# Optimization experiments

Hardware: AMD Instinct MI355X
Metric: run time of the kernel (lower is better)

The kernel has to match this reference:

```python
import jax, jax.numpy as jnp
import numpy as np

N_NODES = 50000


def _spmm(edge_index, edge_vals, dense):
    """Sparse [N,N] @ dense [N,D] via gather + segment-sum.
    edge_index[0] = row (dst), edge_index[1] = col (src)."""
    dst, src = edge_index[0], edge_index[1]
    msgs = edge_vals[:, None] * dense[src]  # [E, D]
    return jax.ops.segment_sum(msgs, dst, num_segments=N_NODES)


def setup_inputs() -> dict:
    key = jax.random.key(0)
    ks = jax.random.split(key, 8)
    N, D_IN, D_OUT, E = N_NODES, 128, 128, 800000
    x = jax.random.normal(ks[0], (N, D_IN), dtype=jnp.float32)
    # glorot init for weights
    scale = jnp.sqrt(6.0 / (D_IN + D_OUT)).astype(jnp.float32)
    W0 = jax.random.uniform(ks[1], (D_IN, D_OUT), jnp.float32, -scale, scale)
    W1 = jax.random.uniform(ks[2], (D_IN, D_OUT), jnp.float32, -scale, scale)
    bias = jnp.zeros((D_OUT,), dtype=jnp.float32)
    edge_vals0 = jax.random.uniform(ks[3], (E,), dtype=jnp.float32)
    edge_vals1 = jax.random.uniform(ks[4], (E,), dtype=jnp.float32)
    edge_index0 = jax.random.randint(ks[5], (2, E), 0, N, dtype=jnp.int32)
    edge_index1 = jax.random.randint(ks[6], (2, E), 0, N, dtype=jnp.int32)
    return {"x": x, "W0": W0, "W1": W1, "bias": bias,
            "edge_vals0": edge_vals0, "edge_vals1": edge_vals1,
            "edge_index0": edge_index0, "edge_index1": edge_index1}


def reference(x, W0, W1, bias, edge_vals0, edge_vals1, edge_index0, edge_index1):
    # dropout with rate 0 == identity (self.dropout unset in source snippet)
    pre0 = x @ W0  # [N, D_out]
    pre1 = x @ W1
    out = _spmm(edge_index0, edge_vals0, pre0) + _spmm(edge_index1, edge_vals1, pre1)
    out = out + bias
    return jax.nn.relu(out)
```

## Files before the change

### kernel.cpp

```cpp
#include <hip/hip_runtime.h>
#include <hip/hip_bf16.h>


#define BROWS 32
#define NBUCK 1563
#define BCAP 704
#define ACAP (2 * BCAP)
#define FT 4096
#define PREROWS 65536

typedef __attribute__((ext_vector_type(8))) short bf16x8;
typedef __attribute__((ext_vector_type(4))) float f32x4;

__device__ inline unsigned short f2bf(float f) {
    union { float f; unsigned u; } v; v.f = f;
    unsigned r = v.u + 0x7fff + ((v.u >> 16) & 1);
    return (unsigned short)(r >> 16);
}

__global__ __launch_bounds__(256) void convert_w_kernel(
    const float* __restrict__ W0, const float* __restrict__ W1,
    unsigned short* __restrict__ wt0, unsigned short* __restrict__ wt1,
    int* __restrict__ cur, int ncur)
{
    if (blockIdx.x >= 2) {
        int half = (ncur + 1) / 2;
        int base = (blockIdx.x - 2) * half;
        for (int i = threadIdx.x; i < half; i += 256)
            if (base + i < ncur) cur[base + i] = 0;
        return;
    }
    const float* __restrict__ W = blockIdx.x ? W1 : W0;
    unsigned short* __restrict__ wt = blockIdx.x ? wt1 : wt0;
    for (int i = threadIdx.x; i < 128 * 128; i += 256) {
        int k = i >> 7, n = i & 127;
        wt[n * 128 + k] = f2bf(W[i]);
    }
}

__global__ __launch_bounds__(512) void gemm_fused_kernel(
    const float* __restrict__ x,
    const unsigned short* __restrict__ wt0,
    const unsigned short* __restrict__ wt1,
    unsigned short* __restrict__ pre,
    int N)
{
    __shared__ short ctile[8][16][40];

    const int w = threadIdx.x >> 6;
    const int lane = threadIdx.x & 63;
    const int adj = w >> 2;
    const int wq = w & 3;
    const int m0 = blockIdx.x * 16;
    const unsigned short* __restrict__ wt = adj ? wt1 : wt0;
    unsigned short* __restrict__ po = pre + (size_t)adj * PREROWS * 128;
    const int l15 = lane & 15;
    const int quad = lane >> 4;
    const int nA = wq * 32 + l15;

    f32x4 c0 = {0.f, 0.f, 0.f, 0.f};
    f32x4 c1 = {0.f, 0.f, 0.f, 0.f};
#pragma unroll
    for (int k0 = 0; k0 < 128; k0 += 32) {
        const float* xp = &x[(m0 + l15) * 128 + k0 + quad * 8];
        float4 v0 = *(const float4*)xp;
        float4 v1 = *(const float4*)(xp + 4);
        bf16x8 a;
        ((short*)&a)[0] = (short)f2bf(v0.x);
        ((short*)&a)[1] = (short)f2bf(v0.y);
        ((short*)&a)[2] = (short)f2bf(v0.z);
        ((short*)&a)[3] = (short)f2bf(v0.w);
        ((short*)&a)[4] = (short)f2bf(v1.x);
        ((short*)&a)[5] = (short)f2bf(v1.y);
        ((short*)&a)[6] = (short)f2bf(v1.z);
        ((short*)&a)[7] = (short)f2bf(v1.w);
        bf16x8 b0 = *(const bf16x8*)&wt[nA * 128 + k0 + quad * 8];
        bf16x8 b1 = *(const bf16x8*)&wt[(nA + 16) * 128 + k0 + quad * 8];
        c0 = __builtin_amdgcn_mfma_f32_16x16x32_bf16(a, b0, c0, 0, 0, 0);
        c1 = __builtin_amdgcn_mfma_f32_16x16x32_bf16(a, b1, c1, 0, 0, 0);
    }

#pragma unroll
    for (int i = 0; i < 4; ++i) {
        ctile[w][quad * 4 + i][l15]      = (short)f2bf(c0[i]);
        ctile[w][quad * 4 + i][16 + l15] = (short)f2bf(c1[i]);
    }
    const int rr = lane >> 2, cg = (lane & 3) * 8;
    ushort4 s0 = *(ushort4*)&ctile[w][rr][cg];
    ushort4 s1 = *(ushort4*)&ctile[w][rr][cg + 4];
    int row = m0 + rr;
    *(ushort4*)&po[row * 128 + wq * 32 + cg] = s0;
    *(ushort4*)&po[row * 128 + wq * 32 + cg + 4] = s1;
}

__global__ __launch_bounds__(1024) void fill4_kernel(
    const int* __restrict__ ei0, const int* __restrict__ ei1,
    const float* __restrict__ ev0, const float* __restrict__ ev1,
    int* __restrict__ cur, int2* __restrict__ recs, int E)
{
    const int a = blockIdx.y;
    const int* __restrict__ ei = a ? ei1 : ei0;
    const float* __restrict__ ev = a ? ev1 : ev0;

    __shared__ int lcnt[NBUCK];
    __shared__ int gbase[NBUCK];
    __shared__ int glim[NBUCK];
    for (int k = threadIdx.x; k < NBUCK; k += 1024) lcnt[k] = 0;
    __syncthreads();

    const int e0 = blockIdx.x * FT;
    unsigned ds[4];
    float val[4];
    short rank[4];
#pragma unroll
    for (int j = 0; j < 4; ++j) {
        int e = e0 + j * 1024 + threadIdx.x;
        if (e < E) {
            int d = ei[e];
            int s = ei[E + e];
            ds[j] = ((unsigned)d << 16) | (unsigned)s;
            val[j] = ev[e];
            rank[j] = (short)atomicAdd(&lcnt[d >> 5], 1);
        } else ds[j] = 0xffffffffu;
    }
    __syncthreads();

    for (int k = threadIdx.x; k < NBUCK; k += 1024) {
        int c = lcnt[k];
        int base = 0, lim = 0;
        if (c > 0) {
            int bin = k * 2 + a;
            int b0 = atomicAdd(&cur[bin], c);
            lim = BCAP - b0; if (lim < 0) lim = 0;
            base = bin * BCAP + b0;
        }
        gbase[k] = base;
        glim[k] = lim;
    }
    __syncthreads();

#pragma unroll
    for (int j = 0; j < 4; ++j) {
        if (ds[j] != 0xffffffffu) {
            int key = ds[j] >> 21;
            int r = rank[j];
            if (r < glim[key]) {
                int rl = (ds[j] >> 16) & 31;
                recs[gbase[key] + r] =
                    make_int2((rl << 17) | (a << 16) | (ds[j] & 0xffff),
                              __float_as_int(val[j]));
            }
        }
    }
}

__global__ __launch_bounds__(256, 6) void aggregate9_kernel(
    const int* __restrict__ cur, const int2* __restrict__ recs,
    const unsigned short* __restrict__ pre,
    const float* __restrict__ bias,
    float* __restrict__ out, int N)
{
    __shared__ int2 srec[ACAP];
    __shared__ int2 srt[ACAP];
    __shared__ int lcnt[32];
    __shared__ int lstart[32];
    __shared__ int lcur[32];

    const int b = blockIdx.x;
    const int tid = threadIdx.x;

    int n0 = cur[2 * b];     if (n0 > BCAP) n0 = BCAP;
    int n1 = cur[2 * b + 1]; if (n1 > BCAP) n1 = BCAP;
    const int total = n0 + n1;
    const int base0 = (2 * b) * BCAP, base1 = (2 * b + 1) * BCAP;

    if (tid < 32) lcnt[tid] = 0;
    __syncthreads();

    for (int i = tid; i < total; i += 256) {
        int2 r = (i < n0) ? recs[base0 + i] : recs[base1 + i - n0];
        srec[i] = r;
        atomicAdd(&lcnt[(r.x >> 17) & 31], 1);
    }
    __syncthreads();

    if (tid < 32) {
        int cme = lcnt[tid];
        int p = cme;
#pragma unroll
        for (int o = 1; o < 32; o <<= 1) {
            int t = __shfl_up(p, o);
            if (tid >= o) p += t;
        }
        lstart[tid] = p - cme;
        lcur[tid] = p - cme;
    }
    __syncthreads();

    for (int i = tid; i < total; i += 256) {
        int2 r = srec[i];
        srt[atomicAdd(&lcur[(r.x >> 17) & 31], 1)] = r;
    }
    __syncthreads();

    const int wv = tid >> 6;
    const int lane = tid & 63;
    const float2 bi = *(const float2*)&bias[lane * 2];

#define GA(r) (*(const unsigned*)&pre[((r).x & 0x1ffff) * 128 + 2 * lane])
#define ACC(r, u) { float v = __int_as_float((r).y);                    \
        acc.x = fmaf(v, __uint_as_float((u) << 16), acc.x);             \
        acc.y = fmaf(v, __uint_as_float((u) & 0xffff0000u), acc.y); }

    for (int t = 0; t < 8; ++t) {
        const int rl = wv * 8 + t;
        const int s = lstart[rl];
        const int e = s + lcnt[rl];
        float2 acc = make_float2(0.f, 0.f);
        int j = s;
        for (; j + 8 <= e; j += 8) {
            int2 r0 = srt[j], r1 = srt[j + 1], r2 = srt[j + 2], r3 = srt[j + 3];
            int2 r4 = srt[j + 4], r5 = srt[j + 5], r6 = srt[j + 6], r7 = srt[j + 7];
            unsigned u0 = GA(r0), u1 = GA(r1), u2 = GA(r2), u3 = GA(r3);
            unsigned u4 = GA(r4), u5 = GA(r5), u6 = GA(r6), u7 = GA(r7);
            ACC(r0, u0); ACC(r1, u1); ACC(r2, u2); ACC(r3, u3);
            ACC(r4, u4); ACC(r5, u5); ACC(r6, u6); ACC(r7, u7);
        }
        for (; j + 4 <= e; j += 4) {
            int2 r0 = srt[j], r1 = srt[j + 1], r2 = srt[j + 2], r3 = srt[j + 3];
            unsigned u0 = GA(r0), u1 = GA(r1), u2 = GA(r2), u3 = GA(r3);
            ACC(r0, u0); ACC(r1, u1); ACC(r2, u2); ACC(r3, u3);
        }
        for (; j < e; ++j) {
            int2 r0 = srt[j];
            unsigned u0 = GA(r0);
            ACC(r0, u0);
        }
        int row = b * BROWS + rl;
        if (row < N) {
            float2 o;
            o.x = fmaxf(acc.x + bi.x, 0.f);
            o.y = fmaxf(acc.y + bi.y, 0.f);
            *(float2*)&out[row * 128 + 2 * lane] = o;
        }
    }
#undef GA
#undef ACC
}

extern "C" void kernel_launch(void* const* d_in, const int* in_sizes, int n_in,
                              void* d_out, int out_size, void* d_ws, size_t ws_size,
                              hipStream_t stream) {
    const float* x    = (const float*)d_in[0];
    const float* W0   = (const float*)d_in[1];
    const float* W1   = (const float*)d_in[2];
    const float* bias = (const float*)d_in[3];
    const float* ev0  = (const float*)d_in[4];
    const float* ev1  = (const float*)d_in[5];
    const int*   ei0  = (const int*)d_in[6];
    const int*   ei1  = (const int*)d_in[7];
    float* out = (float*)d_out;

    const int N = in_sizes[0] / 128;
    const int E = in_sizes[4];
    const int NBINS2 = NBUCK * 2;

    char* w = (char*)d_ws;
    unsigned short* pre = (unsigned short*)w;   w += (size_t)2 * PREROWS * 128 * 2;
    unsigned short* wt0 = (unsigned short*)w;   w += (size_t)128 * 128 * 2;
    unsigned short* wt1 = (unsigned short*)w;   w += (size_t)128 * 128 * 2;
    int* cur = (int*)w;                         w += (size_t)NBINS2 * 4;
    int2* recs = (int2*)w;                      w += (size_t)NBINS2 * BCAP * 8;

    convert_w_kernel<<<4, 256, 0, stream>>>(W0, W1, wt0, wt1, cur, NBINS2);

    gemm_fused_kernel<<<N / 16, 512, 0, stream>>>(x, wt0, wt1, pre, N);

    dim3 fgrid((E + FT - 1) / FT, 2);
    fill4_kernel<<<fgrid, 1024, 0, stream>>>(ei0, ei1, ev0, ev1, cur, recs, E);

    aggregate9_kernel<<<NBUCK, 256, 0, stream>>>(cur, recs, pre, bias, out, N);
}
```

Before: 239.0 us.

## Pre-convert x to bf16 in a separate pass and enlarge fill tile size

Adds a pass to the setup kernel that converts x to bf16 once into a workspace buffer. The GEMM then loads bf16 directly, so the two weight-column-group waves that each read and converted the same fp32 rows no longer duplicate that work. It also raises the fill kernel's edges per block from 4096 to 16384, which cuts the number of blocks and global bucket atomics but raises per-thread register use and lowers parallelism. The cost is an extra full read of x and a write plus re-read of the bf16 copy.

```diff
diff --git a/kernel.cpp b/kernel.cpp
--- a/kernel.cpp
+++ b/kernel.cpp
@@ -6,7 +6,7 @@
 #define NBUCK 1563
 #define BCAP 704
 #define ACAP (2 * BCAP)
-#define FT 4096
+#define FT 16384
 #define PREROWS 65536
 
 typedef __attribute__((ext_vector_type(8))) short bf16x8;
@@ -18,28 +18,43 @@
     return (unsigned short)(r >> 16);
 }
 
-__global__ __launch_bounds__(256) void convert_w_kernel(
-    const float* __restrict__ W0, const float* __restrict__ W1,
+__global__ __launch_bounds__(256) void convert_kernel(
+    const float* __restrict__ x, const float* __restrict__ W0,
+    const float* __restrict__ W1,
+    unsigned short* __restrict__ xb,
     unsigned short* __restrict__ wt0, unsigned short* __restrict__ wt1,
-    int* __restrict__ cur, int ncur)
-{
-    if (blockIdx.x >= 2) {
-        int half = (ncur + 1) / 2;
-        int base = (blockIdx.x - 2) * half;
-        for (int i = threadIdx.x; i < half; i += 256)
-            if (base + i < ncur) cur[base + i] = 0;
+    int* __restrict__ cur, int ncur, int nxb, int nx4)
+{
+    int bid = blockIdx.x;
+    int tid = threadIdx.x;
+    if (bid < nxb) {
+        int i4 = bid * 256 + tid;
+        if (i4 < nx4) {
+            float4 v = *(const float4*)&x[i4 * 4];
+            ushort4 s;
+            s.x = f2bf(v.x); s.y = f2bf(v.y); s.z = f2bf(v.z); s.w = f2bf(v.w);
+            *(ushort4*)&xb[i4 * 4] = s;
+        }
         return;
     }
-    const float* __restrict__ W = blockIdx.x ? W1 : W0;
-    unsigned short* __restrict__ wt = blockIdx.x ? wt1 : wt0;
-    for (int i = threadIdx.x; i < 128 * 128; i += 256) {
-        int k = i >> 7, n = i & 127;
-        wt[n * 128 + k] = f2bf(W[i]);
-    }
+    int r = bid - nxb;
+    if (r < 2) {
+        const float* __restrict__ W = r ? W1 : W0;
+        unsigned short* __restrict__ wt = r ? wt1 : wt0;
+        for (int i = tid; i < 128 * 128; i += 256) {
+            int k = i >> 7, n = i & 127;
+            wt[n * 128 + k] = f2bf(W[i]);
+        }
+        return;
+    }
+    int half = (ncur + 1) / 2;
+    int base = (r - 2) * half;
+    for (int i = tid; i < half; i += 256)
+        if (base + i < ncur) cur[base + i] = 0;
 }
 
 __global__ __launch_bounds__(512) void gemm_fused_kernel(
-    const float* __restrict__ x,
+    const unsigned short* __restrict__ xb,
     const unsigned short* __restrict__ wt0,
     const unsigned short* __restrict__ wt1,
     unsigned short* __restrict__ pre,
@@ -62,18 +77,7 @@
     f32x4 c1 = {0.f, 0.f, 0.f, 0.f};
 #pragma unroll
     for (int k0 = 0; k0 < 128; k0 += 32) {
-        const float* xp = &x[(m0 + l15) * 128 + k0 + quad * 8];
-        float4 v0 = *(const float4*)xp;
-        float4 v1 = *(const float4*)(xp + 4);
-        bf16x8 a;
-        ((short*)&a)[0] = (short)f2bf(v0.x);
-        ((short*)&a)[1] = (short)f2bf(v0.y);
-        ((short*)&a)[2] = (short)f2bf(v0.z);
-        ((short*)&a)[3] = (short)f2bf(v0.w);
-        ((short*)&a)[4] = (short)f2bf(v1.x);
-        ((short*)&a)[5] = (short)f2bf(v1.y);
-        ((short*)&a)[6] = (short)f2bf(v1.z);
-        ((short*)&a)[7] = (short)f2bf(v1.w);
+        bf16x8 a  = *(const bf16x8*)&xb[(m0 + l15) * 128 + k0 + quad * 8];
         bf16x8 b0 = *(const bf16x8*)&wt[nA * 128 + k0 + quad * 8];
         bf16x8 b1 = *(const bf16x8*)&wt[(nA + 16) * 128 + k0 + quad * 8];
         c0 = __builtin_amdgcn_mfma_f32_16x16x32_bf16(a, b0, c0, 0, 0, 0);
@@ -109,11 +113,11 @@
     __syncthreads();
 
     const int e0 = blockIdx.x * FT;
-    unsigned ds[4];
-    float val[4];
-    short rank[4];
-#pragma unroll
-    for (int j = 0; j < 4; ++j) {
+    unsigned ds[16];
+    float val[16];
+    short rank[16];
+#pragma unroll
+    for (int j = 0; j < 16; ++j) {
         int e = e0 + j * 1024 + threadIdx.x;
         if (e < E) {
             int d = ei[e];
@@ -140,7 +144,7 @@
     __syncthreads();
 
 #pragma unroll
-    for (int j = 0; j < 4; ++j) {
+    for (int j = 0; j < 16; ++j) {
         if (ds[j] != 0xffffffffu) {
             int key = ds[j] >> 21;
             int r = rank[j];
@@ -263,18 +267,23 @@
 
     const int N = in_sizes[0] / 128;
     const int E = in_sizes[4];
+    const int NX = N * 128;
     const int NBINS2 = NBUCK * 2;
 
     char* w = (char*)d_ws;
     unsigned short* pre = (unsigned short*)w;   w += (size_t)2 * PREROWS * 128 * 2;
+    unsigned short* xb  = (unsigned short*)w;   w += (size_t)NX * 2;
     unsigned short* wt0 = (unsigned short*)w;   w += (size_t)128 * 128 * 2;
     unsigned short* wt1 = (unsigned short*)w;   w += (size_t)128 * 128 * 2;
     int* cur = (int*)w;                         w += (size_t)NBINS2 * 4;
     int2* recs = (int2*)w;                      w += (size_t)NBINS2 * BCAP * 8;
 
-    convert_w_kernel<<<4, 256, 0, stream>>>(W0, W1, wt0, wt1, cur, NBINS2);
-
-    gemm_fused_kernel<<<N / 16, 512, 0, stream>>>(x, wt0, wt1, pre, N);
+    const int nx4 = NX / 4;
+    const int nxb = (nx4 + 255) / 256;
+    convert_kernel<<<nxb + 4, 256, 0, stream>>>(x, W0, W1, xb, wt0, wt1,
+                                                cur, NBINS2, nxb, nx4);
+
+    gemm_fused_kernel<<<N / 16, 512, 0, stream>>>(xb, wt0, wt1, pre, N);
 
     dim3 fgrid((E + FT - 1) / FT, 2);
     fill4_kernel<<<fgrid, 1024, 0, stream>>>(ei0, ei1, ev0, ev1, cur, recs, E);
```

Result: faster. 233.4 us (-2.4%).

## Locally sort edges in shared memory before bucket scatter; stage x in LDS

Applied to the files above, without the earlier changes.

The fill kernel now handles 8192 edges per block. It counts them per bucket, prefix-scans the counts, and sorts the records in shared memory. It then writes them to the global bucket bins with contiguous, coalesced stores instead of scattered per-edge writes. The GEMM kernel converts each x tile to bf16 once into LDS instead of having every wave reload and convert it, and the weight-transpose prep is split over more blocks. The cost is heavy LDS use in the fill kernel (~110KB at 1024 threads), which limits it to one block per CU, plus an extra serial scan and barrier.

```diff
diff --git a/kernel.cpp b/kernel.cpp
--- a/kernel.cpp
+++ b/kernel.cpp
@@ -4,9 +4,10 @@
 
 #define BROWS 32
 #define NBUCK 1563
+#define NB2 2048
 #define BCAP 704
 #define ACAP (2 * BCAP)
-#define FT 4096
+#define FT5 8192
 #define PREROWS 65536
 
 typedef __attribute__((ext_vector_type(8))) short bf16x8;
@@ -18,23 +19,24 @@
     return (unsigned short)(r >> 16);
 }
 
-__global__ __launch_bounds__(256) void convert_w_kernel(
+__global__ __launch_bounds__(256) void prep_kernel(
     const float* __restrict__ W0, const float* __restrict__ W1,
     unsigned short* __restrict__ wt0, unsigned short* __restrict__ wt1,
     int* __restrict__ cur, int ncur)
 {
-    if (blockIdx.x >= 2) {
-        int half = (ncur + 1) / 2;
-        int base = (blockIdx.x - 2) * half;
-        for (int i = threadIdx.x; i < half; i += 256)
-            if (base + i < ncur) cur[base + i] = 0;
+    const int bid = blockIdx.x;
+    const int tid = threadIdx.x;
+    if (bid >= 8) {
+        for (int i = tid; i < ncur; i += 256) cur[i] = 0;
         return;
     }
-    const float* __restrict__ W = blockIdx.x ? W1 : W0;
-    unsigned short* __restrict__ wt = blockIdx.x ? wt1 : wt0;
-    for (int i = threadIdx.x; i < 128 * 128; i += 256) {
-        int k = i >> 7, n = i & 127;
-        wt[n * 128 + k] = f2bf(W[i]);
+    const int which = bid >> 2;
+    const int k0 = (bid & 3) * 32;
+    const float* __restrict__ W = which ? W1 : W0;
+    unsigned short* __restrict__ wt = which ? wt1 : wt0;
+    for (int i = tid; i < 32 * 128; i += 256) {
+        int k = k0 + (i >> 7), n = i & 127;
+        wt[n * 128 + k] = f2bf(W[k * 128 + n]);
     }
 }
 
@@ -45,13 +47,26 @@
     unsigned short* __restrict__ pre,
     int N)
 {
+    __shared__ unsigned short sA[16][136];
     __shared__ short ctile[8][16][40];
 
-    const int w = threadIdx.x >> 6;
-    const int lane = threadIdx.x & 63;
+    const int tid = threadIdx.x;
+    const int m0 = blockIdx.x * 16;
+
+    {
+        int r = tid >> 5;
+        int c4 = (tid & 31) << 2;
+        float4 v = *(const float4*)&x[(m0 + r) * 128 + c4];
+        ushort4 s;
+        s.x = f2bf(v.x); s.y = f2bf(v.y); s.z = f2bf(v.z); s.w = f2bf(v.w);
+        *(ushort4*)&sA[r][c4] = s;
+    }
+    __syncthreads();
+
+    const int w = tid >> 6;
+    const int lane = tid & 63;
     const int adj = w >> 2;
     const int wq = w & 3;
-    const int m0 = blockIdx.x * 16;
     const unsigned short* __restrict__ wt = adj ? wt1 : wt0;
     unsigned short* __restrict__ po = pre + (size_t)adj * PREROWS * 128;
     const int l15 = lane & 15;
@@ -62,22 +77,13 @@
     f32x4 c1 = {0.f, 0.f, 0.f, 0.f};
 #pragma unroll
     for (int k0 = 0; k0 < 128; k0 += 32) {
-        const float* xp = &x[(m0 + l15) * 128 + k0 + quad * 8];
-        float4 v0 = *(const float4*)xp;
-        float4 v1 = *(const float4*)(xp + 4);
-        bf16x8 a;
-        ((short*)&a)[0] = (short)f2bf(v0.x);
-        ((short*)&a)[1] = (short)f2bf(v0.y);
-        ((short*)&a)[2] = (short)f2bf(v0.z);
-        ((short*)&a)[3] = (short)f2bf(v0.w);
-        ((short*)&a)[4] = (short)f2bf(v1.x);
-        ((short*)&a)[5] = (short)f2bf(v1.y);
-        ((short*)&a)[6] = (short)f2bf(v1.z);
-        ((short*)&a)[7] = (short)f2bf(v1.w);
+        union { bf16x8 v; ushort4 h[2]; } au;
+        au.h[0] = *(const ushort4*)&sA[l15][k0 + quad * 8];
+        au.h[1] = *(const ushort4*)&sA[l15][k0 + quad * 8 + 4];
         bf16x8 b0 = *(const bf16x8*)&wt[nA * 128 + k0 + quad * 8];
         bf16x8 b1 = *(const bf16x8*)&wt[(nA + 16) * 128 + k0 + quad * 8];
-        c0 = __builtin_amdgcn_mfma_f32_16x16x32_bf16(a, b0, c0, 0, 0, 0);
-        c1 = __builtin_amdgcn_mfma_f32_16x16x32_bf16(a, b1, c1, 0, 0, 0);
+        c0 = __builtin_amdgcn_mfma_f32_16x16x32_bf16(au.v, b0, c0, 0, 0, 0);
+        c1 = __builtin_amdgcn_mfma_f32_16x16x32_bf16(au.v, b1, c1, 0, 0, 0);
     }
 
 #pragma unroll
@@ -93,64 +99,88 @@
     *(ushort4*)&po[row * 128 + wq * 32 + cg + 4] = s1;
 }
 
-__global__ __launch_bounds__(1024) void fill4_kernel(
+__global__ __launch_bounds__(1024) void fill5_kernel(
     const int* __restrict__ ei0, const int* __restrict__ ei1,
     const float* __restrict__ ev0, const float* __restrict__ ev1,
     int* __restrict__ cur, int2* __restrict__ recs, int E)
 {
+    __shared__ int2 srt[FT5];
+    __shared__ unsigned short skey[FT5];
+    __shared__ int lcnt[NB2];
+    __shared__ int bstart[NB2];
+    __shared__ int lcur[NB2];
+    __shared__ int gpos[NBUCK];
+    __shared__ int glim[NBUCK];
+    __shared__ int part[1024];
+
     const int a = blockIdx.y;
     const int* __restrict__ ei = a ? ei1 : ei0;
     const float* __restrict__ ev = a ? ev1 : ev0;
-
-    __shared__ int lcnt[NBUCK];
-    __shared__ int gbase[NBUCK];
-    __shared__ int glim[NBUCK];
-    for (int k = threadIdx.x; k < NBUCK; k += 1024) lcnt[k] = 0;
-    __syncthreads();
-
-    const int e0 = blockIdx.x * FT;
-    unsigned ds[4];
-    float val[4];
-    short rank[4];
-#pragma unroll
-    for (int j = 0; j < 4; ++j) {
-        int e = e0 + j * 1024 + threadIdx.x;
+    const int tid = threadIdx.x;
+    const int e0 = blockIdx.x * FT5;
+
+    lcnt[tid] = 0; lcnt[tid + 1024] = 0;
+    __syncthreads();
+
+    int2 rec[8];
+    int key8[8];
+#pragma unroll
+    for (int j = 0; j < 8; ++j) {
+        int e = e0 + j * 1024 + tid;
         if (e < E) {
             int d = ei[e];
             int s = ei[E + e];
-            ds[j] = ((unsigned)d << 16) | (unsigned)s;
-            val[j] = ev[e];
-            rank[j] = (short)atomicAdd(&lcnt[d >> 5], 1);
-        } else ds[j] = 0xffffffffu;
-    }
-    __syncthreads();
-
-    for (int k = threadIdx.x; k < NBUCK; k += 1024) {
-        int c = lcnt[k];
-        int base = 0, lim = 0;
-        if (c > 0) {
+            key8[j] = d >> 5;
+            rec[j] = make_int2(((d & 31) << 17) | (a << 16) | s,
+                               __float_as_int(ev[e]));
+            atomicAdd(&lcnt[key8[j]], 1);
+        } else key8[j] = -1;
+    }
+    __syncthreads();
+
+    int c0 = lcnt[2 * tid], c1 = lcnt[2 * tid + 1];
+    int tsum = c0 + c1;
+    part[tid] = tsum;
+    __syncthreads();
+    for (int o = 1; o < 1024; o <<= 1) {
+        int t = (tid >= o) ? part[tid - o] : 0;
+        __syncthreads();
+        part[tid] += t;
+        __syncthreads();
+    }
+    int run = part[tid] - tsum;
+    const int total = part[1023];
+    bstart[2 * tid] = run; lcur[2 * tid] = run;
+    bstart[2 * tid + 1] = run + c0; lcur[2 * tid + 1] = run + c0;
+
+#pragma unroll
+    for (int h = 0; h < 2; ++h) {
+        int k = 2 * tid + h;
+        int c = h ? c1 : c0;
+        if (k < NBUCK && c > 0) {
             int bin = k * 2 + a;
-            int b0 = atomicAdd(&cur[bin], c);
-            lim = BCAP - b0; if (lim < 0) lim = 0;
-            base = bin * BCAP + b0;
-        }
-        gbase[k] = base;
-        glim[k] = lim;
-    }
-    __syncthreads();
-
-#pragma unroll
-    for (int j = 0; j < 4; ++j) {
-        if (ds[j] != 0xffffffffu) {
-            int key = ds[j] >> 21;
-            int r = rank[j];
-            if (r < glim[key]) {
-                int rl = (ds[j] >> 16) & 31;
-                recs[gbase[key] + r] =
-                    make_int2((rl << 17) | (a << 16) | (ds[j] & 0xffff),
-                              __float_as_int(val[j]));
-            }
-        }
+            int g = atomicAdd(&cur[bin], c);
+            int lim = BCAP - g; if (lim < 0) lim = 0;
+            gpos[k] = bin * BCAP + g;
+            glim[k] = lim;
+        }
+    }
+    __syncthreads();
+
+#pragma unroll
+    for (int j = 0; j < 8; ++j) {
+        if (key8[j] >= 0) {
+            int p = atomicAdd(&lcur[key8[j]], 1);
+            srt[p] = rec[j];
+            skey[p] = (unsigned short)key8[j];
+        }
+    }
+    __syncthreads();
+
+    for (int i = tid; i < total; i += 1024) {
+        int k = skey[i];
+        int r = i - bstart[k];
+        if (r < glim[k]) recs[gpos[k] + r] = srt[i];
     }
 }
 
@@ -272,12 +302,12 @@
     int* cur = (int*)w;                         w += (size_t)NBINS2 * 4;
     int2* recs = (int2*)w;                      w += (size_t)NBINS2 * BCAP * 8;
 
-    convert_w_kernel<<<4, 256, 0, stream>>>(W0, W1, wt0, wt1, cur, NBINS2);
+    prep_kernel<<<9, 256, 0, stream>>>(W0, W1, wt0, wt1, cur, NBINS2);
 
     gemm_fused_kernel<<<N / 16, 512, 0, stream>>>(x, wt0, wt1, pre, N);
 
-    dim3 fgrid((E + FT - 1) / FT, 2);
-    fill4_kernel<<<fgrid, 1024, 0, stream>>>(ei0, ei1, ev0, ev1, cur, recs, E);
+    dim3 fgrid((E + FT5 - 1) / FT5, 2);
+    fill5_kernel<<<fgrid, 1024, 0, stream>>>(ei0, ei1, ev0, ev1, cur, recs, E);
 
     aggregate9_kernel<<<NBUCK, 256, 0, stream>>>(cur, recs, pre, bias, out, N);
 }
```

After: 201.3 us. 15.8% less time.
